# Optimization experiments

Hardware: AMD Instinct MI355X
Metric: run time of the kernel (lower is better)

## Reference

```python
import jax, jax.numpy as jnp
import numpy as np

EPS = 1e-15

def setup_inputs() -> dict:
    key = jax.random.key(0)
    k1, k2, k3 = jax.random.split(key, 3)
    B, N, F, C = 8, 2048, 256, 64
    x = jax.random.normal(k1, (B, N, F), dtype=jnp.float32)
    adj = jax.random.uniform(k2, (B, N, N), dtype=jnp.float32)
    mask = jnp.ones((B, N), dtype=bool)
    W = jax.random.normal(k3, (F, C), dtype=jnp.float32) * 0.05
    b = jnp.zeros((C,), dtype=jnp.float32)
    return {"x": x, "adj": adj, "mask": mask, "W": W, "b": b}


def reference(x, adj, mask, W, b):
    B, N, F = x.shape
    C = W.shape[1]
    # MLP (single linear, no act/norm), dropout=0 (eval), softmax
    s = jax.nn.softmax(x @ W + b, axis=-1)                 # [B,N,C]
    m_f = mask.astype(x.dtype)[..., None]                  # [B,N,1]
    x = x * m_f
    s = s * m_f
    st = jnp.swapaxes(s, 1, 2)                             # [B,C,N]
    out = jax.nn.selu(st @ x)                              # [B,C,F]
    out_adj = st @ adj @ s                                 # [B,C,C]
    degrees = jnp.sum(adj, axis=-1)[..., None] * m_f       # [B,N,1]
    m = jnp.sum(degrees, axis=(1, 2)) / 2                  # [B]
    ca = st @ degrees                                      # [B,C,1]
    cb = jnp.swapaxes(degrees, 1, 2) @ s                   # [B,1,C]
    normalizer = (ca @ cb) / 2 / m[:, None, None]          # [B,C,C]
    decompose = out_adj - normalizer
    spectral_loss = jnp.mean(-jnp.trace(decompose, axis1=-2, axis2=-1) / 2 / m)
    ss = st @ s                                            # [B,C,C]
    i_s = jnp.eye(C, dtype=ss.dtype)
    ss_n = jnp.linalg.norm(ss, axis=(-2, -1), keepdims=True)
    i_n = jnp.linalg.norm(i_s)                             # sqrt(C)
    ortho_loss = jnp.mean(jnp.linalg.norm(ss / ss_n - i_s / i_n, axis=(-2, -1)))
    cluster_size = jnp.sum(s, axis=1)                      # [B,C]
    # note: torch broadcasts [B] / [B,1] -> [B,B]; reproduce faithfully
    cl = jnp.linalg.norm(cluster_size, axis=1) / jnp.sum(m_f, axis=1) * i_n - 1
    cluster_loss = jnp.mean(cl)
    ind = jnp.arange(C)
    out_adj = out_adj.at[:, ind, ind].set(0.0)
    d = jnp.sqrt(jnp.sum(out_adj, axis=-1))[:, None] + EPS  # [B,1,C]
    out_adj = out_adj / d / jnp.swapaxes(d, 1, 2)
    return (s, out, out_adj, spectral_loss, ortho_loss, cluster_loss)
```

## Files before the change

### kernel.cpp

```cpp
#include <hip/hip_runtime.h>
#include <math.h>

#define NB 8
#define NN 2048
#define NF 256
#define NC 64

typedef short bf16x8 __attribute__((ext_vector_type(8)));
typedef float f32x4  __attribute__((ext_vector_type(4)));

#define OFF_S    0
#define OFF_OUT  (NB*NN*NC)
#define OFF_OADJ (OFF_OUT + NB*NC*NF)
#define OFF_SCAL (OFF_OADJ + NB*NC*NC)

#define WS_T    0
#define WS_DEG  (2*NB*NN*NC)
#define WS_SF   (WS_DEG + 4*NB*NN)
#define WS_POUT (WS_SF + NB*32*8*64*4)
#define WS_PADJ (WS_POUT + NB*4*16*4096)
#define WS_PSS  (WS_PADJ + NB*32*4096)
#define WS_PCS  (WS_PSS  + NB*32*4096)
#define WS_RADJ (WS_PCS  + NB*32*64)
#define WS_RSS  (WS_RADJ + NB*4096)
#define WS_RCS  (WS_RSS  + NB*4096)
#define WS_BS   (WS_RCS  + NB*64)

__device__ __forceinline__ unsigned short f2bf(float f) {
    union { float f; unsigned int u; } v; v.f = f;
    unsigned int u = v.u;
    return (unsigned short)((u + 0x7FFFu + ((u >> 16) & 1u)) >> 16);
}
__device__ __forceinline__ float bf2f(unsigned short h) {
    union { unsigned int u; float f; } v; v.u = ((unsigned int)h) << 16;
    return v.f;
}

__global__ __launch_bounds__(512) void k_fused_s(
    const float* __restrict__ x, const float* __restrict__ W,
    const float* __restrict__ bias, float* __restrict__ s_out,
    unsigned short* __restrict__ sfrag, float* __restrict__ P_ss,
    float* __restrict__ P_cs)
{
    const int ch = blockIdx.x & 31;
    const int b  = blockIdx.x >> 5;
    const int n0 = ch * 64;
    __shared__ float xs[64][260];
    __shared__ float sB[64][68];
    __shared__ float csP[8][68];
    const int t = threadIdx.x, w = t >> 6, l = t & 63;
    const float* X = x + ((size_t)b * NN + n0) * NF;

    #pragma unroll
    for (int r = 0; r < 8; ++r) {
        const int row = w * 8 + r;
        *(float4*)&xs[row][l * 4] = *(const float4*)&X[(size_t)row * NF + l * 4];
    }
    const float bz = bias[l];
    float acc[8];
    #pragma unroll
    for (int r = 0; r < 8; ++r) acc[r] = bz;
    #pragma unroll 4
    for (int k4 = 0; k4 < 64; ++k4) {
        const int k = k4 * 4;
        const float w0 = W[(k + 0) * NC + l], w1 = W[(k + 1) * NC + l],
                    w2 = W[(k + 2) * NC + l], w3 = W[(k + 3) * NC + l];
        #pragma unroll
        for (int r = 0; r < 8; ++r) {
            const float4 xv = *(const float4*)&xs[w * 8 + r][k];
            acc[r] = fmaf(xv.x, w0, acc[r]); acc[r] = fmaf(xv.y, w1, acc[r]);
            acc[r] = fmaf(xv.z, w2, acc[r]); acc[r] = fmaf(xv.w, w3, acc[r]);
        }
    }
    float cs_acc = 0.f;
    #pragma unroll
    for (int r = 0; r < 8; ++r) {
        float a = acc[r], mx = a;
        #pragma unroll
        for (int off = 32; off; off >>= 1) mx = fmaxf(mx, __shfl_xor(mx, off));
        const float e = __expf(a - mx);
        float sum = e;
        #pragma unroll
        for (int off = 32; off; off >>= 1) sum += __shfl_xor(sum, off);
        const float sv = e / sum;
        s_out[((size_t)b * NN + n0 + w * 8 + r) * NC + l] = sv;
        sB[w * 8 + r][l] = sv;
        cs_acc += sv;
    }
    csP[w][l] = cs_acc;
    __syncthreads();

    {
        const int n = w >> 1, kk = w & 1;
        const int col = 16 * n + (l & 15);
        const int kb  = 32 * kk + (l >> 4) * 8;
        unsigned short tmp[8];
        #pragma unroll
        for (int r = 0; r < 8; ++r) tmp[r] = f2bf(sB[kb + r][col]);
        *(uint4*)&sfrag[((((size_t)(b * 32 + ch)) * 8 + w) * 64 + l) * 8] = *(uint4*)tmp;
    }
    {
        const int c0 = (t >> 5) * 4;
        const int c2 = (t & 31) * 2;
        float a2[4][2] = {{0.f,0.f},{0.f,0.f},{0.f,0.f},{0.f,0.f}};
        #pragma unroll 8
        for (int n = 0; n < 64; ++n) {
            const float4 av = *(const float4*)&sB[n][c0];
            const float2 bv = *(const float2*)&sB[n][c2];
            const float av_[4] = {av.x, av.y, av.z, av.w};
            #pragma unroll
            for (int i = 0; i < 4; ++i) {
                a2[i][0] = fmaf(av_[i], bv.x, a2[i][0]);
                a2[i][1] = fmaf(av_[i], bv.y, a2[i][1]);
            }
        }
        float* Ps = P_ss + (size_t)(b * 32 + ch) * 4096;
        #pragma unroll
        for (int i = 0; i < 4; ++i) {
            float2 v; v.x = a2[i][0]; v.y = a2[i][1];
            *(float2*)&Ps[(c0 + i) * 64 + c2] = v;
        }
    }
    if (t < 64) {
        float v = 0.f;
        #pragma unroll
        for (int g = 0; g < 8; ++g) v += csP[g][t];
        P_cs[(b * 32 + ch) * 64 + t] = v;
    }
}

__global__ __launch_bounds__(256, 4) void k_adj_reg(
    const float* __restrict__ adj, const unsigned short* __restrict__ sfrag,
    unsigned short* __restrict__ Tbuf4, float* __restrict__ deg4)
{
    const int h  = blockIdx.x & 3;
    const int mt = (blockIdx.x >> 2) & 31;
    const int b  = blockIdx.x >> 7;
    const int m0 = mt * 64;
    const int t = threadIdx.x, w = t >> 6, l = t & 63;
    const int row = m0 + 16 * w + (l & 15);
    const float* Arow = adj + (size_t)b * NN * NN + (size_t)row * NN + h * 512 + (l >> 4) * 8;
    const unsigned short* BF = sfrag + ((size_t)(b * 32 + h * 8)) * 8 * 64 * 8 + (size_t)l * 8;

    f32x4 acc[4] = {};
    float dsum = 0.f;
    float4 a0 = *(const float4*)&Arow[0];
    float4 a1 = *(const float4*)&Arow[4];
    #pragma unroll 2
    for (int ks = 0; ks < 16; ++ks) {
        float4 p0v = a0, p1v = a1;
        if (ks < 15) {
            p0v = *(const float4*)&Arow[(ks + 1) * 32];
            p1v = *(const float4*)&Arow[(ks + 1) * 32 + 4];
        }
        dsum += a0.x + a0.y + a0.z + a0.w + a1.x + a1.y + a1.z + a1.w;
        unsigned q0, q1, q2, q3;
        asm("v_cvt_pk_bf16_f32 %0, %1, %2" : "=v"(q0) : "v"(a0.x), "v"(a0.y));
        asm("v_cvt_pk_bf16_f32 %0, %1, %2" : "=v"(q1) : "v"(a0.z), "v"(a0.w));
        asm("v_cvt_pk_bf16_f32 %0, %1, %2" : "=v"(q2) : "v"(a1.x), "v"(a1.y));
        asm("v_cvt_pk_bf16_f32 %0, %1, %2" : "=v"(q3) : "v"(a1.z), "v"(a1.w));
        uint4 af_u; af_u.x = q0; af_u.y = q1; af_u.z = q2; af_u.w = q3;
        const bf16x8 af = *(const bf16x8*)&af_u;
        const unsigned short* Bk = BF + ((size_t)((ks >> 1) * 8 + (ks & 1))) * 64 * 8;
        #pragma unroll
        for (int n = 0; n < 4; ++n) {
            const bf16x8 bfv = *(const bf16x8*)&Bk[(size_t)(n * 2) * 64 * 8];
            acc[n] = __builtin_amdgcn_mfma_f32_16x16x32_bf16(af, bfv, acc[n], 0, 0, 0);
        }
        a0 = p0v; a1 = p1v;
    }
    unsigned short* Tw = Tbuf4 + (((size_t)b * NN + m0 + 16 * w) * 4 + h) * 64;
    #pragma unroll
    for (int n = 0; n < 4; ++n)
        #pragma unroll
        for (int j = 0; j < 4; ++j)
            Tw[(size_t)((l >> 4) * 4 + j) * 256 + n * 16 + (l & 15)] = f2bf(acc[n][j]);
    dsum += __shfl_xor(dsum, 16);
    dsum += __shfl_xor(dsum, 32);
    if (l < 16)
        deg4[(size_t)(h * NB + b) * NN + m0 + 16 * w + l] = dsum;
}

__global__ __launch_bounds__(256) void k_stx(
    const float* __restrict__ x, const float* __restrict__ s,
    float* __restrict__ P_out)
{
    const int ch = blockIdx.x & 15;
    const int ft = (blockIdx.x >> 4) & 3;
    const int b  = blockIdx.x >> 6;

    __shared__ float sL[64][68];
    __shared__ float xL[64][68];

    const int t  = threadIdx.x;
    const int lr = t >> 6;
    const int lc = t & 63;
    const int tr = t >> 4;
    const int tc = t & 15;
    const int r0 = tr * 4, c0 = tc * 4;

    const float* S = s + (size_t)b * NN * NC;
    const float* X = x + (size_t)b * NN * NF + ft * 64;

    float acc[4][4] = {{0.f,0.f,0.f,0.f},{0.f,0.f,0.f,0.f},{0.f,0.f,0.f,0.f},{0.f,0.f,0.f,0.f}};

    for (int tile = 0; tile < 2; ++tile) {
        const int nb = ch * 128 + tile * 64;
        __syncthreads();
        #pragma unroll
        for (int k = 0; k < 16; ++k) {
            const int nn = lr + 4 * k;
            sL[nn][lc] = S[(size_t)(nb + nn) * NC + lc];
            xL[nn][lc] = X[(size_t)(nb + nn) * NF + lc];
        }
        __syncthreads();
        #pragma unroll 8
        for (int n = 0; n < 64; ++n) {
            const float4 av = *(const float4*)&sL[n][r0];
            const float4 bv = *(const float4*)&xL[n][c0];
            const float av_[4] = {av.x, av.y, av.z, av.w};
            const float bv_[4] = {bv.x, bv.y, bv.z, bv.w};
            #pragma unroll
            for (int i = 0; i < 4; ++i)
                #pragma unroll
                for (int j = 0; j < 4; ++j)
                    acc[i][j] = fmaf(av_[i], bv_[j], acc[i][j]);
        }
    }
    float* P = P_out + (size_t)blockIdx.x * 4096;
    #pragma unroll
    for (int i = 0; i < 4; ++i) {
        float4 v; v.x = acc[i][0]; v.y = acc[i][1]; v.z = acc[i][2]; v.w = acc[i][3];
        *(float4*)&P[(r0 + i) * 64 + c0] = v;
    }
}

__global__ __launch_bounds__(256) void k_red_cc(
    const float* __restrict__ s, const unsigned short* __restrict__ Tbuf4,
    float* __restrict__ P_adj)
{
    const int ch = blockIdx.x & 31;
    const int b  = blockIdx.x >> 5;
    const int nb = ch * 64;

    __shared__ float sL[64][68];
    __shared__ float tL[64][68];

    const int t  = threadIdx.x;
    const int lr = t >> 6;
    const int lc = t & 63;
    const int tr = t >> 4;
    const int tc = t & 15;
    const int r0 = tr * 4, c0 = tc * 4;

    const float* S = s + (size_t)b * NN * NC;

    float aadj[4][4] = {{0.f,0.f,0.f,0.f},{0.f,0.f,0.f,0.f},{0.f,0.f,0.f,0.f},{0.f,0.f,0.f,0.f}};

    #pragma unroll
    for (int k = 0; k < 16; ++k) {
        const int nn = lr + 4 * k;
        sL[nn][lc] = S[(size_t)(nb + nn) * NC + lc];
        const unsigned short* Tp = &Tbuf4[(((size_t)b * NN + nb + nn) * 4) * 64 + lc];
        tL[nn][lc] = bf2f(Tp[0]) + bf2f(Tp[64]) + bf2f(Tp[128]) + bf2f(Tp[192]);
    }
    __syncthreads();
    #pragma unroll 8
    for (int n = 0; n < 64; ++n) {
        const float4 av = *(const float4*)&sL[n][r0];
        const float4 tv = *(const float4*)&tL[n][c0];
        const float av_[4] = {av.x, av.y, av.z, av.w};
        const float tv_[4] = {tv.x, tv.y, tv.z, tv.w};
        #pragma unroll
        for (int i = 0; i < 4; ++i)
            #pragma unroll
            for (int j = 0; j < 4; ++j)
                aadj[i][j] = fmaf(av_[i], tv_[j], aadj[i][j]);
    }
    float* Pa = P_adj + (size_t)(b * 32 + ch) * 4096;
    #pragma unroll
    for (int i = 0; i < 4; ++i) {
        float4 v; v.x = aadj[i][0]; v.y = aadj[i][1]; v.z = aadj[i][2]; v.w = aadj[i][3];
        *(float4*)&Pa[(r0 + i) * 64 + c0] = v;
    }
}

__global__ __launch_bounds__(256) void k_reduce2(
    const float* __restrict__ Pout, const float* __restrict__ P_adj,
    const float* __restrict__ P_ss, const float* __restrict__ P_cs,
    float* __restrict__ out, float* __restrict__ Radj, float* __restrict__ Rss,
    float* __restrict__ Rcs)
{
    const int bid = blockIdx.x;
    const int t = threadIdx.x;
    if (bid < 512) {
        const int idx = bid * 256 + t;
        const int f  = idx & 255;
        const int cc = (idx >> 8) & 63;
        const int b  = idx >> 14;
        const int ft = f >> 6, ff = f & 63;
        const float* P = Pout + ((size_t)(b * 4 + ft) * 16) * 4096 + cc * 64 + ff;
        float v = 0.f;
        #pragma unroll
        for (int ch = 0; ch < 16; ++ch) v += P[(size_t)ch * 4096];
        const float scale = 1.0507009873554805f, alpha = 1.6732632423543772f;
        out[idx] = (v > 0.f) ? scale * v : scale * alpha * expm1f(v);
    } else if (bid < 768) {
        const int idx = (bid - 512) * 256 + t;
        const int arr = idx >> 15;
        const int rem = idx & 32767;
        const int b   = rem >> 12;
        const int e   = rem & 4095;
        const float* P = (arr == 0 ? P_adj : P_ss) + (size_t)(b * 32) * 4096 + e;
        float v = 0.f;
        #pragma unroll
        for (int ch = 0; ch < 32; ++ch) v += P[(size_t)ch * 4096];
        (arr == 0 ? Radj : Rss)[b * 4096 + e] = v;
    } else {
        for (int e = t; e < 512; e += 256) {
            const int b = e >> 6, c = e & 63;
            const float* P = P_cs + (size_t)(b * 32) * 64 + c;
            float v = 0.f;
            #pragma unroll
            for (int ch = 0; ch < 32; ++ch) v += P[ch * 64];
            Rcs[b * 64 + c] = v;
        }
    }
}

__device__ __forceinline__ float block_sum(float v, float* red)
{
    #pragma unroll
    for (int off = 32; off; off >>= 1) v += __shfl_xor(v, off);
    const int w = threadIdx.x >> 6;
    __syncthreads();
    if ((threadIdx.x & 63) == 0) red[w] = v;
    __syncthreads();
    return red[0] + red[1] + red[2] + red[3];
}

__global__ __launch_bounds__(256) void k_finalize(
    const float* __restrict__ Radj, const float* __restrict__ Rss,
    const float* __restrict__ Rcs, const float* __restrict__ deg4,
    const float* __restrict__ s,
    float* __restrict__ oadj_out, float* __restrict__ bscal)
{
    const int b = blockIdx.x;
    const int t = threadIdx.x;
    __shared__ float oadj[64][65];
    __shared__ float ssm [64][65];
    __shared__ float degL[NN];
    __shared__ float caP[16][68];
    __shared__ float ca[64], cs[64], dd[64];
    __shared__ float red[4];

    for (int e = t; e < 4096; e += 256) {
        const int i = e >> 6, j = e & 63;
        oadj[i][j] = Radj[(size_t)b * 4096 + e];
        ssm [i][j] = Rss [(size_t)b * 4096 + e];
    }
    if (t < 64) cs[t] = Rcs[b * 64 + t];

    float dsum = 0.f;
    for (int n = t; n < NN; n += 256) {
        float dv = 0.f;
        #pragma unroll
        for (int p = 0; p < 4; ++p)
            dv += deg4[(size_t)(p * NB + b) * NN + n];
        degL[n] = dv;
        dsum += dv;
    }
    const float m = 0.5f * block_sum(dsum, red);

    {
        const int c4 = (t & 15) * 4;
        const int g  = t >> 4;
        const float* S = s + (size_t)b * NN * NC;
        float cacc[4] = {0.f, 0.f, 0.f, 0.f};
        for (int i = 0; i < 128; ++i) {
            const int n = g * 128 + i;
            const float4 sv = *(const float4*)&S[(size_t)n * NC + c4];
            const float dv = degL[n];
            cacc[0] = fmaf(sv.x, dv, cacc[0]);
            cacc[1] = fmaf(sv.y, dv, cacc[1]);
            cacc[2] = fmaf(sv.z, dv, cacc[2]);
            cacc[3] = fmaf(sv.w, dv, cacc[3]);
        }
        #pragma unroll
        for (int j = 0; j < 4; ++j) caP[g][c4 + j] = cacc[j];
        __syncthreads();
        if (t < 64) {
            float v = 0.f;
            #pragma unroll
            for (int g2 = 0; g2 < 16; ++g2) v += caP[g2][t];
            ca[t] = v;
        }
    }

    float tv = (t < 64) ? oadj[t][t] : 0.f;
    const float tr_oadj = block_sum(tv, red);
    float cv = (t < 64) ? ca[t] * ca[t] : 0.f;
    const float ca2 = block_sum(cv, red);

    float ss2p = 0.f;
    for (int e = t; e < 4096; e += 256) {
        const float q = ssm[e >> 6][e & 63];
        ss2p += q * q;
    }
    const float ssn = sqrtf(block_sum(ss2p, red));
    float op = 0.f;
    for (int e = t; e < 4096; e += 256) {
        const int i = e >> 6, j = e & 63;
        const float d0 = ssm[i][j] / ssn - ((i == j) ? 0.125f : 0.f);
        op += d0 * d0;
    }
    const float ortho_b = sqrtf(block_sum(op, red));
    float c2 = (t < 64) ? cs[t] * cs[t] : 0.f;
    const float cnorm_b = sqrtf(block_sum(c2, red));

    if (t == 0) {
        const float trn = ca2 / (2.f * m);
        bscal[b]          = -(tr_oadj - trn) / (2.f * m);
        bscal[NB + b]     = ortho_b;
        bscal[2 * NB + b] = cnorm_b;
    }

    __syncthreads();
    if (t < 64) oadj[t][t] = 0.f;
    __syncthreads();
    if (t < 64) {
        float rs = 0.f;
        #pragma unroll 8
        for (int j = 0; j < 64; ++j) rs += oadj[t][j];
        dd[t] = sqrtf(rs) + 1e-15f;
    }
    __syncthreads();
    float* O = oadj_out + (size_t)b * 4096;
    for (int e = t; e < 4096; e += 256) {
        const int i = e >> 6, j = e & 63;
        O[e] = oadj[i][j] / (dd[i] * dd[j]);
    }
}

__global__ void k_scalars(const float* __restrict__ bscal, float* __restrict__ scal_out)
{
    if (threadIdx.x == 0 && blockIdx.x == 0) {
        float sp = 0.f, orth = 0.f, cn = 0.f;
        for (int b = 0; b < NB; ++b) {
            sp   += bscal[b];
            orth += bscal[NB + b];
            cn   += bscal[2 * NB + b];
        }
        scal_out[0] = sp / NB;
        scal_out[1] = orth / NB;
        scal_out[2] = (cn / NB) * 8.0f / 2048.0f - 1.0f;
    }
}

extern "C" void kernel_launch(void* const* d_in, const int* in_sizes, int n_in,
                              void* d_out, int out_size, void* d_ws, size_t ws_size,
                              hipStream_t stream)
{
    const float* x    = (const float*)d_in[0];
    const float* adj  = (const float*)d_in[1];
    const float* W    = (const float*)d_in[3];
    const float* bias = (const float*)d_in[4];

    float* out = (float*)d_out;
    float* ws  = (float*)d_ws;

    float*          s_out = out + OFF_S;
    unsigned short* Tbuf4 = (unsigned short*)(ws + WS_T);
    float*          deg4  = ws + WS_DEG;
    unsigned short* sfrag = (unsigned short*)(ws + WS_SF);
    float*          Pout  = ws + WS_POUT;
    float*          Padj  = ws + WS_PADJ;
    float*          Pss   = ws + WS_PSS;
    float*          Pcs   = ws + WS_PCS;
    float*          Radj  = ws + WS_RADJ;
    float*          Rss   = ws + WS_RSS;
    float*          Rcs   = ws + WS_RCS;
    float*          bscal = ws + WS_BS;

    k_fused_s <<<NB * 32,     512, 0, stream>>>(x, W, bias, s_out, sfrag, Pss, Pcs);
    k_adj_reg <<<NB * 32 * 4, 256, 0, stream>>>(adj, sfrag, Tbuf4, deg4);
    k_stx     <<<NB * 4 * 16, 256, 0, stream>>>(x, s_out, Pout);
    k_red_cc  <<<NB * 32,     256, 0, stream>>>(s_out, Tbuf4, Padj);
    k_reduce2 <<<769,         256, 0, stream>>>(Pout, Padj, Pss, Pcs,
                                                out + OFF_OUT, Radj, Rss, Rcs);
    k_finalize<<<NB,          256, 0, stream>>>(Radj, Rss, Rcs, deg4, s_out,
                                                out + OFF_OADJ, bscal);
    k_scalars <<<1, 64, 0, stream>>>(bscal, out + OFF_SCAL);
}
```

Before: 89.81 us.

## Merge adj and stx kernels, stage adj via LDS DMA, move ca into redmix

Merges the adj·s MFMA kernel and the sᵀx kernel into one launch that dispatches on block index. The adj tiles now go through swizzled, double-buffered LDS using global_load_lds instead of direct register loads. The sᵀ·degree (ca) product moves out of the serial per-batch finalize kernel into the parallel red_cc blocks, with partials reduced in a new reduce kernel. SELU output reduction is also folded into the same launch as red_cc. Together these cut launches and serial work in finalize, at the cost of more LDS traffic and lower occupancy in the adj path.

Result: faster. 79.97 us (-11.0%).

```diff
diff --git a/kernel.cpp b/kernel.cpp
--- a/kernel.cpp
+++ b/kernel.cpp
@@ -18,12 +18,14 @@
 #define WS_DEG  (2*NB*NN*NC)
 #define WS_SF   (WS_DEG + 4*NB*NN)
 #define WS_POUT (WS_SF + NB*32*8*64*4)
-#define WS_PADJ (WS_POUT + NB*4*16*4096)
+#define WS_PADJ (WS_POUT + 512*4096)
 #define WS_PSS  (WS_PADJ + NB*32*4096)
-#define WS_PCS  (WS_PSS  + NB*32*4096)
+#define WS_PCA  (WS_PSS  + NB*32*4096)
+#define WS_PCS  (WS_PCA  + NB*32*64)
 #define WS_RADJ (WS_PCS  + NB*32*64)
 #define WS_RSS  (WS_RADJ + NB*4096)
-#define WS_RCS  (WS_RSS  + NB*4096)
+#define WS_RCA  (WS_RSS  + NB*4096)
+#define WS_RCS  (WS_RCA  + NB*64)
 #define WS_BS   (WS_RCS  + NB*64)
 
 __device__ __forceinline__ unsigned short f2bf(float f) {
@@ -35,6 +37,12 @@
     union { unsigned int u; float f; } v; v.u = ((unsigned int)h) << 16;
     return v.f;
 }
+__device__ __forceinline__ void gload16(const float* g, float* l) {
+    __builtin_amdgcn_global_load_lds(
+        (const __attribute__((address_space(1))) float*)g,
+        (__attribute__((address_space(3))) float*)l, 16, 0, 0);
+}
+__device__ __forceinline__ int swz(int r) { return ((r & 3) << 1) | ((r >> 2) & 1); }
 
 __global__ __launch_bounds__(512) void k_fused_s(
     const float* __restrict__ x, const float* __restrict__ W,
@@ -47,7 +55,7 @@
     const int n0 = ch * 64;
     __shared__ float xs[64][260];
     __shared__ float sB[64][68];
-    __shared__ float csP[8][68];
+    __shared__ float csP[8][64];
     const int t = threadIdx.x, w = t >> 6, l = t & 63;
     const float* X = x + ((size_t)b * NN + n0) * NF;
 
@@ -129,172 +137,194 @@
     }
 }
 
-__global__ __launch_bounds__(256, 4) void k_adj_reg(
+__global__ __launch_bounds__(256) void k_adj_stx(
     const float* __restrict__ adj, const unsigned short* __restrict__ sfrag,
-    unsigned short* __restrict__ Tbuf4, float* __restrict__ deg4)
-{
-    const int h  = blockIdx.x & 3;
-    const int mt = (blockIdx.x >> 2) & 31;
-    const int b  = blockIdx.x >> 7;
-    const int m0 = mt * 64;
-    const int t = threadIdx.x, w = t >> 6, l = t & 63;
-    const int row = m0 + 16 * w + (l & 15);
-    const float* Arow = adj + (size_t)b * NN * NN + (size_t)row * NN + h * 512 + (l >> 4) * 8;
-    const unsigned short* BF = sfrag + ((size_t)(b * 32 + h * 8)) * 8 * 64 * 8 + (size_t)l * 8;
-
-    f32x4 acc[4] = {};
-    float dsum = 0.f;
-    float4 a0 = *(const float4*)&Arow[0];
-    float4 a1 = *(const float4*)&Arow[4];
-    #pragma unroll 2
-    for (int ks = 0; ks < 16; ++ks) {
-        float4 p0v = a0, p1v = a1;
-        if (ks < 15) {
-            p0v = *(const float4*)&Arow[(ks + 1) * 32];
-            p1v = *(const float4*)&Arow[(ks + 1) * 32 + 4];
-        }
-        dsum += a0.x + a0.y + a0.z + a0.w + a1.x + a1.y + a1.z + a1.w;
-        unsigned q0, q1, q2, q3;
-        asm("v_cvt_pk_bf16_f32 %0, %1, %2" : "=v"(q0) : "v"(a0.x), "v"(a0.y));
-        asm("v_cvt_pk_bf16_f32 %0, %1, %2" : "=v"(q1) : "v"(a0.z), "v"(a0.w));
-        asm("v_cvt_pk_bf16_f32 %0, %1, %2" : "=v"(q2) : "v"(a1.x), "v"(a1.y));
-        asm("v_cvt_pk_bf16_f32 %0, %1, %2" : "=v"(q3) : "v"(a1.z), "v"(a1.w));
-        uint4 af_u; af_u.x = q0; af_u.y = q1; af_u.z = q2; af_u.w = q3;
-        const bf16x8 af = *(const bf16x8*)&af_u;
-        const unsigned short* Bk = BF + ((size_t)((ks >> 1) * 8 + (ks & 1))) * 64 * 8;
-        #pragma unroll
-        for (int n = 0; n < 4; ++n) {
-            const bf16x8 bfv = *(const bf16x8*)&Bk[(size_t)(n * 2) * 64 * 8];
-            acc[n] = __builtin_amdgcn_mfma_f32_16x16x32_bf16(af, bfv, acc[n], 0, 0, 0);
-        }
-        a0 = p0v; a1 = p1v;
-    }
-    unsigned short* Tw = Tbuf4 + (((size_t)b * NN + m0 + 16 * w) * 4 + h) * 64;
-    #pragma unroll
-    for (int n = 0; n < 4; ++n)
-        #pragma unroll
-        for (int j = 0; j < 4; ++j)
-            Tw[(size_t)((l >> 4) * 4 + j) * 256 + n * 16 + (l & 15)] = f2bf(acc[n][j]);
-    dsum += __shfl_xor(dsum, 16);
-    dsum += __shfl_xor(dsum, 32);
-    if (l < 16)
-        deg4[(size_t)(h * NB + b) * NN + m0 + 16 * w + l] = dsum;
-}
-
-__global__ __launch_bounds__(256) void k_stx(
     const float* __restrict__ x, const float* __restrict__ s,
+    unsigned short* __restrict__ Tbuf4, float* __restrict__ deg4,
     float* __restrict__ P_out)
 {
-    const int ch = blockIdx.x & 15;
-    const int ft = (blockIdx.x >> 4) & 3;
-    const int b  = blockIdx.x >> 6;
-
-    __shared__ float sL[64][68];
-    __shared__ float xL[64][68];
-
-    const int t  = threadIdx.x;
-    const int lr = t >> 6;
-    const int lc = t & 63;
-    const int tr = t >> 4;
-    const int tc = t & 15;
-    const int r0 = tr * 4, c0 = tc * 4;
-
-    const float* S = s + (size_t)b * NN * NC;
-    const float* X = x + (size_t)b * NN * NF + ft * 64;
-
-    float acc[4][4] = {{0.f,0.f,0.f,0.f},{0.f,0.f,0.f,0.f},{0.f,0.f,0.f,0.f},{0.f,0.f,0.f,0.f}};
-
-    for (int tile = 0; tile < 2; ++tile) {
-        const int nb = ch * 128 + tile * 64;
+    __shared__ __align__(16) char smem[34816];
+    const int bid = blockIdx.x;
+    const int t = threadIdx.x;
+    if (bid < 1024) {
+        const int h = bid & 3, mt = (bid >> 2) & 31, b = bid >> 7;
+        const int m0 = mt * 64;
+        const int w = t >> 6, l = t & 63;
+        float* aL = (float*)smem;
+
+        const float* Ab = adj + (size_t)b * NN * NN + (size_t)m0 * NN + h * 512;
+        const unsigned short* BF = sfrag + ((size_t)(b * 32 + h * 8)) * 8 * 64 * 8
+                                 + (size_t)l * 8;
+
+        size_t goff[4]; int loff[4];
+        #pragma unroll
+        for (int u = 0; u < 4; ++u) {
+            const int r  = 16 * w + 4 * u + (l >> 4);
+            const int gg = ((l & 15) >> 1) ^ swz(r);
+            goff[u] = (size_t)r * NN + gg * 8 + (l & 1) * 4;
+            loff[u] = (16 * w + 4 * u) * 64;
+        }
+
+        f32x4 acc[4] = {};
+        float dsum = 0.f;
+
+        #pragma unroll
+        for (int u = 0; u < 4; ++u)
+            gload16(Ab + goff[u], &aL[loff[u]]);
         __syncthreads();
+
+        const int row = 16 * w + (l & 15);
+        const int swrow = swz(row);
+
+        for (int step = 0; step < 8; ++step) {
+            if (step < 7) {
+                const float* An = Ab + (step + 1) * 64;
+                float* dst = aL + ((step + 1) & 1) * 4096;
+                #pragma unroll
+                for (int u = 0; u < 4; ++u)
+                    gload16(An + goff[u], &dst[loff[u]]);
+            }
+            const float* buf = aL + (step & 1) * 4096;
+            bf16x8 afrag[2];
+            #pragma unroll
+            for (int kk = 0; kk < 2; ++kk) {
+                const int slot = (kk * 4 + (l >> 4)) ^ swrow;
+                const float4 f0 = *(const float4*)&buf[row * 64 + slot * 8];
+                const float4 f1 = *(const float4*)&buf[row * 64 + slot * 8 + 4];
+                dsum += f0.x + f0.y + f0.z + f0.w + f1.x + f1.y + f1.z + f1.w;
+                unsigned q0, q1, q2, q3;
+                asm("v_cvt_pk_bf16_f32 %0, %1, %2" : "=v"(q0) : "v"(f0.x), "v"(f0.y));
+                asm("v_cvt_pk_bf16_f32 %0, %1, %2" : "=v"(q1) : "v"(f0.z), "v"(f0.w));
+                asm("v_cvt_pk_bf16_f32 %0, %1, %2" : "=v"(q2) : "v"(f1.x), "v"(f1.y));
+                asm("v_cvt_pk_bf16_f32 %0, %1, %2" : "=v"(q3) : "v"(f1.z), "v"(f1.w));
+                uint4 afu; afu.x = q0; afu.y = q1; afu.z = q2; afu.w = q3;
+                afrag[kk] = *(const bf16x8*)&afu;
+            }
+            #pragma unroll
+            for (int n = 0; n < 4; ++n) {
+                const bf16x8 b0 = *(const bf16x8*)&BF[((size_t)step * 8 + 2 * n) * 512];
+                const bf16x8 b1 = *(const bf16x8*)&BF[((size_t)step * 8 + 2 * n + 1) * 512];
+                acc[n] = __builtin_amdgcn_mfma_f32_16x16x32_bf16(afrag[0], b0, acc[n], 0, 0, 0);
+                acc[n] = __builtin_amdgcn_mfma_f32_16x16x32_bf16(afrag[1], b1, acc[n], 0, 0, 0);
+            }
+            __syncthreads();
+        }
+
+        unsigned short* Tw = Tbuf4 + (((size_t)b * NN + m0 + 16 * w) * 4 + h) * 64;
+        #pragma unroll
+        for (int n = 0; n < 4; ++n)
+            #pragma unroll
+            for (int j = 0; j < 4; ++j)
+                Tw[(size_t)((l >> 4) * 4 + j) * 256 + n * 16 + (l & 15)] = f2bf(acc[n][j]);
+
+        dsum += __shfl_xor(dsum, 16);
+        dsum += __shfl_xor(dsum, 32);
+        if (l < 16)
+            deg4[(size_t)(h * NB + b) * NN + m0 + 16 * w + l] = dsum;
+    } else {
+        const int sb = bid - 1024;
+        const int ch = sb & 15, ft = (sb >> 4) & 3, b = sb >> 6;
+        float (*sL)[68] = (float(*)[68])smem;
+        float (*xL)[68] = (float(*)[68])(smem + 17408);
+        const int lr = t >> 6, lc = t & 63;
+        const int r0 = (t >> 4) * 4, c0 = (t & 15) * 4;
+        const float* S = s + (size_t)b * NN * NC;
+        const float* X = x + (size_t)b * NN * NF + ft * 64;
+        float acc[4][4] = {{0,0,0,0},{0,0,0,0},{0,0,0,0},{0,0,0,0}};
+        for (int tile = 0; tile < 2; ++tile) {
+            const int nb = ch * 128 + tile * 64;
+            __syncthreads();
+            #pragma unroll
+            for (int k = 0; k < 16; ++k) {
+                const int nn = lr + 4 * k;
+                sL[nn][lc] = S[(size_t)(nb + nn) * NC + lc];
+                xL[nn][lc] = X[(size_t)(nb + nn) * NF + lc];
+            }
+            __syncthreads();
+            #pragma unroll 8
+            for (int n = 0; n < 64; ++n) {
+                const float4 av = *(const float4*)&sL[n][r0];
+                const float4 bv = *(const float4*)&xL[n][c0];
+                const float av_[4] = {av.x, av.y, av.z, av.w};
+                const float bv_[4] = {bv.x, bv.y, bv.z, bv.w};
+                #pragma unroll
+                for (int i = 0; i < 4; ++i)
+                    #pragma unroll
+                    for (int j = 0; j < 4; ++j)
+                        acc[i][j] = fmaf(av_[i], bv_[j], acc[i][j]);
+            }
+        }
+        float* P = P_out + (size_t)sb * 4096;
+        #pragma unroll
+        for (int i = 0; i < 4; ++i) {
+            float4 v; v.x = acc[i][0]; v.y = acc[i][1]; v.z = acc[i][2]; v.w = acc[i][3];
+            *(float4*)&P[(r0 + i) * 64 + c0] = v;
+        }
+    }
+}
+
+__global__ __launch_bounds__(256) void k_redmix(
+    const float* __restrict__ s, const unsigned short* __restrict__ Tbuf4,
+    const float* __restrict__ deg4, const float* __restrict__ Pout,
+    float* __restrict__ P_adj, float* __restrict__ P_ca, float* __restrict__ out)
+{
+    const int bid = blockIdx.x;
+    const int t = threadIdx.x;
+    if (bid < 256) {
+        const int ch = bid & 31, b = bid >> 5;
+        const int nb = ch * 64;
+        __shared__ float sL[64][68];
+        __shared__ float tL[64][68];
+        __shared__ float dL[64];
+        const int lr = t >> 6, lc = t & 63;
+        const int tr = t >> 4, tc = t & 15;
+        const int r0 = tr * 4, c0 = tc * 4;
+        const float* S = s + (size_t)b * NN * NC;
+        float aadj[4][4] = {{0,0,0,0},{0,0,0,0},{0,0,0,0},{0,0,0,0}};
+        float aca[4] = {0.f, 0.f, 0.f, 0.f};
         #pragma unroll
         for (int k = 0; k < 16; ++k) {
             const int nn = lr + 4 * k;
             sL[nn][lc] = S[(size_t)(nb + nn) * NC + lc];
-            xL[nn][lc] = X[(size_t)(nb + nn) * NF + lc];
+            const unsigned short* Tp = &Tbuf4[(((size_t)b * NN + nb + nn) * 4) * 64 + lc];
+            tL[nn][lc] = bf2f(Tp[0]) + bf2f(Tp[64]) + bf2f(Tp[128]) + bf2f(Tp[192]);
+        }
+        if (t < 64) {
+            float dv = 0.f;
+            #pragma unroll
+            for (int p = 0; p < 4; ++p)
+                dv += deg4[(size_t)(p * NB + b) * NN + nb + t];
+            dL[t] = dv;
         }
         __syncthreads();
-        #pragma unroll 8
+        #pragma unroll 4
         for (int n = 0; n < 64; ++n) {
             const float4 av = *(const float4*)&sL[n][r0];
-            const float4 bv = *(const float4*)&xL[n][c0];
+            const float4 tv = *(const float4*)&tL[n][c0];
+            const float dv  = dL[n];
             const float av_[4] = {av.x, av.y, av.z, av.w};
-            const float bv_[4] = {bv.x, bv.y, bv.z, bv.w};
-            #pragma unroll
-            for (int i = 0; i < 4; ++i)
+            const float tv_[4] = {tv.x, tv.y, tv.z, tv.w};
+            #pragma unroll
+            for (int i = 0; i < 4; ++i) {
+                aca[i] = fmaf(av_[i], dv, aca[i]);
                 #pragma unroll
                 for (int j = 0; j < 4; ++j)
-                    acc[i][j] = fmaf(av_[i], bv_[j], acc[i][j]);
-        }
-    }
-    float* P = P_out + (size_t)blockIdx.x * 4096;
-    #pragma unroll
-    for (int i = 0; i < 4; ++i) {
-        float4 v; v.x = acc[i][0]; v.y = acc[i][1]; v.z = acc[i][2]; v.w = acc[i][3];
-        *(float4*)&P[(r0 + i) * 64 + c0] = v;
-    }
-}
-
-__global__ __launch_bounds__(256) void k_red_cc(
-    const float* __restrict__ s, const unsigned short* __restrict__ Tbuf4,
-    float* __restrict__ P_adj)
-{
-    const int ch = blockIdx.x & 31;
-    const int b  = blockIdx.x >> 5;
-    const int nb = ch * 64;
-
-    __shared__ float sL[64][68];
-    __shared__ float tL[64][68];
-
-    const int t  = threadIdx.x;
-    const int lr = t >> 6;
-    const int lc = t & 63;
-    const int tr = t >> 4;
-    const int tc = t & 15;
-    const int r0 = tr * 4, c0 = tc * 4;
-
-    const float* S = s + (size_t)b * NN * NC;
-
-    float aadj[4][4] = {{0.f,0.f,0.f,0.f},{0.f,0.f,0.f,0.f},{0.f,0.f,0.f,0.f},{0.f,0.f,0.f,0.f}};
-
-    #pragma unroll
-    for (int k = 0; k < 16; ++k) {
-        const int nn = lr + 4 * k;
-        sL[nn][lc] = S[(size_t)(nb + nn) * NC + lc];
-        const unsigned short* Tp = &Tbuf4[(((size_t)b * NN + nb + nn) * 4) * 64 + lc];
-        tL[nn][lc] = bf2f(Tp[0]) + bf2f(Tp[64]) + bf2f(Tp[128]) + bf2f(Tp[192]);
-    }
-    __syncthreads();
-    #pragma unroll 8
-    for (int n = 0; n < 64; ++n) {
-        const float4 av = *(const float4*)&sL[n][r0];
-        const float4 tv = *(const float4*)&tL[n][c0];
-        const float av_[4] = {av.x, av.y, av.z, av.w};
-        const float tv_[4] = {tv.x, tv.y, tv.z, tv.w};
-        #pragma unroll
-        for (int i = 0; i < 4; ++i)
-            #pragma unroll
-            for (int j = 0; j < 4; ++j)
-                aadj[i][j] = fmaf(av_[i], tv_[j], aadj[i][j]);
-    }
-    float* Pa = P_adj + (size_t)(b * 32 + ch) * 4096;
-    #pragma unroll
-    for (int i = 0; i < 4; ++i) {
-        float4 v; v.x = aadj[i][0]; v.y = aadj[i][1]; v.z = aadj[i][2]; v.w = aadj[i][3];
-        *(float4*)&Pa[(r0 + i) * 64 + c0] = v;
-    }
-}
-
-__global__ __launch_bounds__(256) void k_reduce2(
-    const float* __restrict__ Pout, const float* __restrict__ P_adj,
-    const float* __restrict__ P_ss, const float* __restrict__ P_cs,
-    float* __restrict__ out, float* __restrict__ Radj, float* __restrict__ Rss,
-    float* __restrict__ Rcs)
-{
-    const int bid = blockIdx.x;
-    const int t = threadIdx.x;
-    if (bid < 512) {
-        const int idx = bid * 256 + t;
+                    aadj[i][j] = fmaf(av_[i], tv_[j], aadj[i][j]);
+            }
+        }
+        float* Pa = P_adj + (size_t)(b * 32 + ch) * 4096;
+        #pragma unroll
+        for (int i = 0; i < 4; ++i) {
+            float4 v; v.x = aadj[i][0]; v.y = aadj[i][1]; v.z = aadj[i][2]; v.w = aadj[i][3];
+            *(float4*)&Pa[(r0 + i) * 64 + c0] = v;
+        }
+        if (tc == 0) {
+            #pragma unroll
+            for (int i = 0; i < 4; ++i)
+                P_ca[(b * 32 + ch) * 64 + r0 + i] = aca[i];
+        }
+    } else {
+        const int idx = (bid - 256) * 256 + t;
         const int f  = idx & 255;
         const int cc = (idx >> 8) & 63;
         const int b  = idx >> 14;
@@ -302,28 +332,37 @@
         const float* P = Pout + ((size_t)(b * 4 + ft) * 16) * 4096 + cc * 64 + ff;
         float v = 0.f;
         #pragma unroll
-        for (int ch = 0; ch < 16; ++ch) v += P[(size_t)ch * 4096];
+        for (int ch2 = 0; ch2 < 16; ++ch2) v += P[(size_t)ch2 * 4096];
         const float scale = 1.0507009873554805f, alpha = 1.6732632423543772f;
         out[idx] = (v > 0.f) ? scale * v : scale * alpha * expm1f(v);
-    } else if (bid < 768) {
-        const int idx = (bid - 512) * 256 + t;
-        const int arr = idx >> 15;
-        const int rem = idx & 32767;
-        const int b   = rem >> 12;
-        const int e   = rem & 4095;
-        const float* P = (arr == 0 ? P_adj : P_ss) + (size_t)(b * 32) * 4096 + e;
+    }
+}
+
+__global__ __launch_bounds__(256) void k_reduce3(
+    const float* __restrict__ P_adj, const float* __restrict__ P_ss,
+    const float* __restrict__ P_ca, const float* __restrict__ P_cs,
+    float* __restrict__ Radj, float* __restrict__ Rss,
+    float* __restrict__ Rca, float* __restrict__ Rcs)
+{
+    const int bid = blockIdx.x, t = threadIdx.x;
+    if (bid < 256) {
+        const int idx = bid * 256 + t;
+        const int arr = idx >> 15, rem = idx & 32767;
+        const int b = rem >> 12, e = rem & 4095;
+        const float* P = (arr ? P_ss : P_adj) + (size_t)(b * 32) * 4096 + e;
         float v = 0.f;
         #pragma unroll
         for (int ch = 0; ch < 32; ++ch) v += P[(size_t)ch * 4096];
-        (arr == 0 ? Radj : Rss)[b * 4096 + e] = v;
+        (arr ? Rss : Radj)[b * 4096 + e] = v;
     } else {
-        for (int e = t; e < 512; e += 256) {
-            const int b = e >> 6, c = e & 63;
-            const float* P = P_cs + (size_t)(b * 32) * 64 + c;
+        for (int e = t; e < 1024; e += 256) {
+            const int arr = e >> 9, rem = e & 511;
+            const int b = rem >> 6, c = rem & 63;
+            const float* P = (arr ? P_cs : P_ca) + (size_t)(b * 32) * 64 + c;
             float v = 0.f;
             #pragma unroll
             for (int ch = 0; ch < 32; ++ch) v += P[ch * 64];
-            Rcs[b * 64 + c] = v;
+            (arr ? Rcs : Rca)[b * 64 + c] = v;
         }
     }
 }
@@ -341,16 +380,14 @@
 
 __global__ __launch_bounds__(256) void k_finalize(
     const float* __restrict__ Radj, const float* __restrict__ Rss,
-    const float* __restrict__ Rcs, const float* __restrict__ deg4,
-    const float* __restrict__ s,
+    const float* __restrict__ Rca, const float* __restrict__ Rcs,
+    const float* __restrict__ deg4,
     float* __restrict__ oadj_out, float* __restrict__ bscal)
 {
     const int b = blockIdx.x;
     const int t = threadIdx.x;
     __shared__ float oadj[64][65];
     __shared__ float ssm [64][65];
-    __shared__ float degL[NN];
-    __shared__ float caP[16][68];
     __shared__ float ca[64], cs[64], dd[64];
     __shared__ float red[4];
 
@@ -359,43 +396,18 @@
         oadj[i][j] = Radj[(size_t)b * 4096 + e];
         ssm [i][j] = Rss [(size_t)b * 4096 + e];
     }
-    if (t < 64) cs[t] = Rcs[b * 64 + t];
+    if (t < 64) {
+        ca[t] = Rca[b * 64 + t];
+        cs[t] = Rcs[b * 64 + t];
+    }
 
     float dsum = 0.f;
     for (int n = t; n < NN; n += 256) {
-        float dv = 0.f;
         #pragma unroll
         for (int p = 0; p < 4; ++p)
-            dv += deg4[(size_t)(p * NB + b) * NN + n];
-        degL[n] = dv;
-        dsum += dv;
+            dsum += deg4[(size_t)(p * NB + b) * NN + n];
     }
     const float m = 0.5f * block_sum(dsum, red);
-
-    {
-        const int c4 = (t & 15) * 4;
-        const int g  = t >> 4;
-        const float* S = s + (size_t)b * NN * NC;
-        float cacc[4] = {0.f, 0.f, 0.f, 0.f};
-        for (int i = 0; i < 128; ++i) {
-            const int n = g * 128 + i;
-            const float4 sv = *(const float4*)&S[(size_t)n * NC + c4];
-            const float dv = degL[n];
-            cacc[0] = fmaf(sv.x, dv, cacc[0]);
-            cacc[1] = fmaf(sv.y, dv, cacc[1]);
-            cacc[2] = fmaf(sv.z, dv, cacc[2]);
-            cacc[3] = fmaf(sv.w, dv, cacc[3]);
-        }
-        #pragma unroll
-        for (int j = 0; j < 4; ++j) caP[g][c4 + j] = cacc[j];
-        __syncthreads();
-        if (t < 64) {
-            float v = 0.f;
-            #pragma unroll
-            for (int g2 = 0; g2 < 16; ++g2) v += caP[g2][t];
-            ca[t] = v;
-        }
-    }
 
     float tv = (t < 64) ? oadj[t][t] : 0.f;
     const float tr_oadj = block_sum(tv, red);
@@ -476,19 +488,18 @@
     float*          Pout  = ws + WS_POUT;
     float*          Padj  = ws + WS_PADJ;
     float*          Pss   = ws + WS_PSS;
+    float*          Pca   = ws + WS_PCA;
     float*          Pcs   = ws + WS_PCS;
     float*          Radj  = ws + WS_RADJ;
     float*          Rss   = ws + WS_RSS;
+    float*          Rca   = ws + WS_RCA;
     float*          Rcs   = ws + WS_RCS;
     float*          bscal = ws + WS_BS;
 
-    k_fused_s <<<NB * 32,     512, 0, stream>>>(x, W, bias, s_out, sfrag, Pss, Pcs);
-    k_adj_reg <<<NB * 32 * 4, 256, 0, stream>>>(adj, sfrag, Tbuf4, deg4);
-    k_stx     <<<NB * 4 * 16, 256, 0, stream>>>(x, s_out, Pout);
-    k_red_cc  <<<NB * 32,     256, 0, stream>>>(s_out, Tbuf4, Padj);
-    k_reduce2 <<<769,         256, 0, stream>>>(Pout, Padj, Pss, Pcs,
-                                                out + OFF_OUT, Radj, Rss, Rcs);
-    k_finalize<<<NB,          256, 0, stream>>>(Radj, Rss, Rcs, deg4, s_out,
-                                                out + OFF_OADJ, bscal);
+    k_fused_s <<<NB * 32, 512, 0, stream>>>(x, W, bias, s_out, sfrag, Pss, Pcs);
+    k_adj_stx <<<1536,    256, 0, stream>>>(adj, sfrag, x, s_out, Tbuf4, deg4, Pout);
+    k_redmix  <<<768,     256, 0, stream>>>(s_out, Tbuf4, deg4, Pout, Padj, Pca, out + OFF_OUT);
+    k_reduce3 <<<257,     256, 0, stream>>>(Padj, Pss, Pca, Pcs, Radj, Rss, Rca, Rcs);
+    k_finalize<<<NB,      256, 0, stream>>>(Radj, Rss, Rca, Rcs, deg4, out + OFF_OADJ, bscal);
     k_scalars <<<1, 64, 0, stream>>>(bscal, out + OFF_SCAL);
 }
```
